# Performance work log

Hardware: AMD Instinct MI355X
Metric: run time of the kernel (lower is better)

Reference implementation:

```python
import jax, jax.numpy as jnp
import numpy as np

B, C, L, OUT = 64, 256, 4096, 256
EPS = 1e-5


def setup_inputs() -> dict:
    key = jax.random.key(0)
    ks = jax.random.split(key, 8)
    s = 1.0 / np.sqrt(C)
    return {
        "x": jax.random.normal(ks[0], (B, C, L), dtype=jnp.float32),
        "Wq": jax.random.normal(ks[1], (C, C), dtype=jnp.float32) * s,
        "Wk": jax.random.normal(ks[2], (C, C), dtype=jnp.float32) * s,
        "Wv": jax.random.normal(ks[3], (C, C), dtype=jnp.float32) * s,
        "Wc": jax.random.normal(ks[4], (C, C), dtype=jnp.float32) * s,
        "Wout": jax.random.normal(ks[5], (OUT, C), dtype=jnp.float32) * s,
        "gamma": jnp.ones((C,), dtype=jnp.float32),
        "beta": jnp.zeros((C,), dtype=jnp.float32),
    }


def _conv1x1(W, x):
    # 1x1 Conv1d, no bias: (O,C) x (B,C,L) -> (B,O,L)
    return jnp.einsum("oc,bcl->bol", W, x)


def reference(x, Wq, Wk, Wv, Wc, Wout, gamma, beta):
    q = _conv1x1(Wq, x)  # (B,C,L)
    k = _conv1x1(Wk, x)  # (B,C,L)
    v = _conv1x1(Wv, x)  # (B,C,L)
    # batch-wise attention: att[b,d,l] = sum_c q[b,c,l]*k[d,c,l] / sqrt(C)
    att = jnp.einsum("bcl,dcl->bdl", q, k) / jnp.sqrt(jnp.asarray(C, x.dtype))
    att = jax.nn.softmax(att, axis=1)  # softmax over the key-batch axis
    # virt[b,c,l] = sum_d att[b,d,l] * v[d,c,l]
    virt = jnp.einsum("bdl,dcl->bcl", att, v)
    # GroupNorm(1, C): normalize over (C,L) per sample, per-channel affine
    mean = jnp.mean(virt, axis=(1, 2), keepdims=True)
    var = jnp.var(virt, axis=(1, 2), keepdims=True)
    virt = (virt - mean) * jax.lax.rsqrt(var + EPS)
    virt = virt * gamma[None, :, None] + beta[None, :, None]
    virt = jax.nn.relu(virt)
    virt = _conv1x1(Wc, virt)
    # dropout is identity in eval mode
    y = x + virt
    return _conv1x1(Wout, y)
```

## Files before the change

kernel.cpp:

```cpp
#include <hip/hip_runtime.h>


typedef __attribute__((ext_vector_type(8))) short          v8s;
typedef __attribute__((ext_vector_type(8))) unsigned short v8u;
typedef __attribute__((ext_vector_type(4))) float          f32x4;

#define MFMA16(a, b, c) __builtin_amdgcn_mfma_f32_16x16x32_bf16((a), (b), (c), 0, 0, 0)

static __device__ __forceinline__ unsigned short f2bf(float f) {
  union { float f; unsigned u; } v; v.f = f;
  unsigned r = (v.u + 0x7FFFu + ((v.u >> 16) & 1u)) >> 16;
  return (unsigned short)r;
}
static __device__ __forceinline__ float bf2f(unsigned short h) {
  union { unsigned u; float f; } v; v.u = ((unsigned)h) << 16; return v.f;
}

__global__ void k_prep(const float* __restrict__ Wq, const float* __restrict__ Wk,
                       const float* __restrict__ Wv, const float* __restrict__ Wc,
                       const float* __restrict__ Wout,
                       unsigned short* __restrict__ Wtv,
                       unsigned short* __restrict__ Wout2,
                       float* __restrict__ stats) {
  int bid = blockIdx.x, j = threadIdx.x;
  if (bid < 256) {
    int i = bid;
    float acc = 0.f;
    for (int c = 0; c < 256; ++c) acc += Wq[c * 256 + i] * Wk[c * 256 + j];
    Wtv[i * 256 + j] = f2bf(acc * 0.0625f);
    Wtv[(256 + i) * 256 + j] = f2bf(Wv[i * 256 + j]);
  } else if (bid < 512) {
    int o = bid - 256;
    float acc = 0.f;
    for (int c = 0; c < 256; ++c) acc += Wout[o * 256 + c] * Wc[c * 256 + j];
    Wout2[o * 512 + 256 + j] = f2bf(acc);
    Wout2[o * 512 + j] = f2bf(Wout[o * 256 + j]);
  } else {
    stats[(bid - 512) * 256 + j] = 0.f;
  }
}

__global__ void k_transpose(const float* __restrict__ x, unsigned short* __restrict__ Xt) {
  __shared__ float tile[64 * 65];
  int bid = blockIdx.x;
  int b = bid >> 8, cb = (bid >> 6) & 3, lb = bid & 63;
  int c0 = cb * 64, l0 = lb * 64, t = threadIdx.x;
#pragma unroll
  for (int i = 0; i < 4; ++i) {
    int idx = i * 256 + t, r = idx >> 4, ch = idx & 15;
    float4 v = *(const float4*)(x + ((size_t)(b * 256 + c0 + r)) * 4096 + l0 + ch * 4);
    tile[r * 65 + ch * 4 + 0] = v.x; tile[r * 65 + ch * 4 + 1] = v.y;
    tile[r * 65 + ch * 4 + 2] = v.z; tile[r * 65 + ch * 4 + 3] = v.w;
  }
  __syncthreads();
#pragma unroll
  for (int i = 0; i < 2; ++i) {
    int idx = i * 256 + t, r = idx >> 3, ch = idx & 7;
    v8u o;
#pragma unroll
    for (int j = 0; j < 8; ++j) o[j] = f2bf(tile[(ch * 8 + j) * 65 + r]);
    *(v8u*)(Xt + ((size_t)(b * 4096 + l0 + r)) * 256 + c0 + ch * 8) = o;
  }
}

__global__ __launch_bounds__(512) void k_fused(const unsigned short* __restrict__ Xt,
                                               const unsigned short* __restrict__ Wtv,
                                               unsigned short* __restrict__ Virt,
                                               float* __restrict__ stats) {
  extern __shared__ char smem[];
  unsigned short* Xs  = (unsigned short*)(smem);
  unsigned short* Ts  = (unsigned short*)(smem + 33792);
  unsigned short* VTs = (unsigned short*)(smem + 67584);
  unsigned short* Ps  = (unsigned short*)(smem + 104448);
  float*          Ss  = (float*)(smem + 113664);
  float*          red = (float*)(smem + 130304);
  float*          rowv= (float*)(smem + 131328);

  int l = blockIdx.x, t = threadIdx.x, lane = t & 63, wv = t >> 6;
  int fr = lane & 15, kq = (lane >> 4) * 8, qr = (lane >> 4) * 4;

#pragma unroll
  for (int i = 0; i < 4; ++i) {
    int idx = i * 512 + t, r = idx >> 5, ch = idx & 31;
    *(v8u*)(Xs + r * 264 + ch * 8) = *(const v8u*)(Xt + ((size_t)(r * 4096 + l)) * 256 + ch * 8);
  }
  __syncthreads();

  {
    int n0 = wv * 64;
    f32x4 acc[4][4];
#pragma unroll
    for (int mi = 0; mi < 4; ++mi)
#pragma unroll
      for (int ni = 0; ni < 4; ++ni) acc[mi][ni] = (f32x4){0.f, 0.f, 0.f, 0.f};
#pragma unroll
    for (int kc = 0; kc < 8; ++kc) {
      v8s a[4], b[4];
#pragma unroll
      for (int mi = 0; mi < 4; ++mi) a[mi] = *(const v8s*)(Xs + (mi * 16 + fr) * 264 + kc * 32 + kq);
#pragma unroll
      for (int ni = 0; ni < 4; ++ni)
        b[ni] = *(const v8s*)(Wtv + (n0 + ni * 16 + fr) * 256 + kc * 32 + kq);
#pragma unroll
      for (int mi = 0; mi < 4; ++mi)
#pragma unroll
        for (int ni = 0; ni < 4; ++ni) acc[mi][ni] = MFMA16(a[mi], b[ni], acc[mi][ni]);
    }
    if (wv < 4) {
#pragma unroll
      for (int mi = 0; mi < 4; ++mi)
#pragma unroll
        for (int ni = 0; ni < 4; ++ni)
#pragma unroll
          for (int i = 0; i < 4; ++i)
            Ts[(mi * 16 + qr + i) * 264 + n0 + ni * 16 + fr] = f2bf(acc[mi][ni][i]);
    } else {
#pragma unroll
      for (int mi = 0; mi < 4; ++mi)
#pragma unroll
        for (int ni = 0; ni < 4; ++ni)
#pragma unroll
          for (int i = 0; i < 4; ++i)
            VTs[(n0 - 256 + ni * 16 + fr) * 72 + mi * 16 + qr + i] = f2bf(acc[mi][ni][i]);
    }
  }
  __syncthreads();

  {
    f32x4 acc[2];
    acc[0] = (f32x4){0.f, 0.f, 0.f, 0.f};
    acc[1] = (f32x4){0.f, 0.f, 0.f, 0.f};
    int tid0 = wv * 2;
#pragma unroll
    for (int kc = 0; kc < 8; ++kc) {
#pragma unroll
      for (int j = 0; j < 2; ++j) {
        int mi = (tid0 + j) >> 2, ni = (tid0 + j) & 3;
        v8s a = *(const v8s*)(Xs + (mi * 16 + fr) * 264 + kc * 32 + kq);
        v8s b = *(const v8s*)(Ts + (ni * 16 + fr) * 264 + kc * 32 + kq);
        acc[j] = MFMA16(a, b, acc[j]);
      }
    }
#pragma unroll
    for (int j = 0; j < 2; ++j) {
      int mi = (tid0 + j) >> 2, ni = (tid0 + j) & 3;
#pragma unroll
      for (int i = 0; i < 4; ++i)
        Ss[(mi * 16 + qr + i) * 65 + ni * 16 + fr] = acc[j][i];
    }
  }
  __syncthreads();

  if (t < 256) {
    int r = t >> 2, seg = t & 3;
    float pm = -1e30f;
    for (int j = seg * 16; j < seg * 16 + 16; ++j) pm = fmaxf(pm, Ss[r * 65 + j]);
    red[r * 4 + seg] = pm;
  }
  __syncthreads();
  if (t < 64) rowv[t] = fmaxf(fmaxf(red[t * 4], red[t * 4 + 1]), fmaxf(red[t * 4 + 2], red[t * 4 + 3]));
  __syncthreads();
  if (t < 256) {
    int r = t >> 2, seg = t & 3;
    float m = rowv[r], ps = 0.f;
    for (int j = seg * 16; j < seg * 16 + 16; ++j) {
      float e = __expf(Ss[r * 65 + j] - m);
      Ps[r * 72 + j] = f2bf(e);
      ps += e;
    }
    red[r * 4 + seg] = ps;
  }
  __syncthreads();
  if (t < 64) rowv[t] = 1.f / (red[t * 4] + red[t * 4 + 1] + red[t * 4 + 2] + red[t * 4 + 3]);
  __syncthreads();

  {
    int n0 = wv * 32;
    f32x4 acc[4][2];
#pragma unroll
    for (int mi = 0; mi < 4; ++mi) { acc[mi][0] = (f32x4){0,0,0,0}; acc[mi][1] = (f32x4){0,0,0,0}; }
#pragma unroll
    for (int kc = 0; kc < 2; ++kc) {
      v8s a[4], b[2];
#pragma unroll
      for (int mi = 0; mi < 4; ++mi) a[mi] = *(const v8s*)(Ps + (mi * 16 + fr) * 72 + kc * 32 + kq);
#pragma unroll
      for (int ni = 0; ni < 2; ++ni)
        b[ni] = *(const v8s*)(VTs + (n0 + ni * 16 + fr) * 72 + kc * 32 + kq);
#pragma unroll
      for (int mi = 0; mi < 4; ++mi)
#pragma unroll
        for (int ni = 0; ni < 2; ++ni) acc[mi][ni] = MFMA16(a[mi], b[ni], acc[mi][ni]);
    }
    __syncthreads();
#pragma unroll
    for (int mi = 0; mi < 4; ++mi)
#pragma unroll
      for (int i = 0; i < 4; ++i) {
        float inv = rowv[mi * 16 + qr + i];
#pragma unroll
        for (int ni = 0; ni < 2; ++ni)
          Ts[(mi * 16 + qr + i) * 264 + n0 + ni * 16 + fr] = f2bf(acc[mi][ni][i] * inv);
      }
  }
  __syncthreads();

  {
    int r = t >> 3, seg = t & 7;
    float s = 0.f, s2 = 0.f;
#pragma unroll
    for (int c4 = 0; c4 < 4; ++c4) {
      v8u v = *(const v8u*)(Ts + r * 264 + seg * 32 + c4 * 8);
#pragma unroll
      for (int j = 0; j < 8; ++j) { float f = bf2f(v[j]); s += f; s2 += f * f; }
      *(v8u*)(Virt + ((size_t)(r * 4096 + l)) * 256 + seg * 32 + c4 * 8) = v;
    }
#pragma unroll
    for (int o = 4; o > 0; o >>= 1) { s += __shfl_xor(s, o); s2 += __shfl_xor(s2, o); }
    if (seg == 0) {
      int slot = blockIdx.x & 31;
      atomicAdd(&stats[slot * 128 + r], s);
      atomicAdd(&stats[slot * 128 + 64 + r], s2);
    }
  }
}

__global__ void k_finalize(float* __restrict__ stats) {
  int t = threadIdx.x;
  if (t < 64) {
    float s = 0.f, s2 = 0.f;
    for (int sl = 0; sl < 32; ++sl) { s += stats[sl * 128 + t]; s2 += stats[sl * 128 + 64 + t]; }
    const float inv = 1.f / 1048576.f;
    float m = s * inv;
    float var = s2 * inv - m * m;
    stats[4096 + t] = m;
    stats[4160 + t] = rsqrtf(var + 1e-5f);
  }
}

__global__ void k_gemm_out(const unsigned short* __restrict__ Xt,
                           const unsigned short* __restrict__ Virt,
                           const unsigned short* __restrict__ Wout2,
                           const float* __restrict__ stats,
                           const float* __restrict__ gamma,
                           const float* __restrict__ beta,
                           float* __restrict__ out) {
  __shared__ unsigned short As[64 * 72];
  __shared__ unsigned short Bs[256 * 72];
  int t = threadIdx.x, lane = t & 63, wv = t >> 6;
  size_t t0 = (size_t)blockIdx.x * 64;
  int b = (int)(t0 >> 12);
  float mean = stats[4096 + b], rstd = stats[4160 + b];
  int n0 = wv * 64;
  f32x4 acc[4][4];
#pragma unroll
  for (int mi = 0; mi < 4; ++mi)
#pragma unroll
    for (int ni = 0; ni < 4; ++ni) acc[mi][ni] = (f32x4){0.f, 0.f, 0.f, 0.f};
  for (int kc = 0; kc < 8; ++kc) {
    __syncthreads();
#pragma unroll
    for (int i = 0; i < 2; ++i) {
      int idx = i * 256 + t, r = idx >> 3, ch = idx & 7;
      if (kc < 4) {
        *(v8u*)(As + r * 72 + ch * 8) = *(const v8u*)(Xt + (t0 + r) * 256 + kc * 64 + ch * 8);
      } else {
        v8u v = *(const v8u*)(Virt + (t0 + r) * 256 + (kc - 4) * 64 + ch * 8);
        int cb = (kc - 4) * 64 + ch * 8;
        float4 g0 = *(const float4*)(gamma + cb), g1 = *(const float4*)(gamma + cb + 4);
        float4 bb0 = *(const float4*)(beta + cb), bb1 = *(const float4*)(beta + cb + 4);
        float gs[8] = {g0.x, g0.y, g0.z, g0.w, g1.x, g1.y, g1.z, g1.w};
        float bs[8] = {bb0.x, bb0.y, bb0.z, bb0.w, bb1.x, bb1.y, bb1.z, bb1.w};
        v8u o;
#pragma unroll
        for (int j = 0; j < 8; ++j) {
          float z = (bf2f(v[j]) - mean) * rstd * gs[j] + bs[j];
          o[j] = f2bf(fmaxf(z, 0.f));
        }
        *(v8u*)(As + r * 72 + ch * 8) = o;
      }
    }
#pragma unroll
    for (int i = 0; i < 8; ++i) {
      int idx = i * 256 + t, r = idx >> 3, ch = idx & 7;
      *(v8u*)(Bs + r * 72 + ch * 8) = *(const v8u*)(Wout2 + r * 512 + kc * 64 + ch * 8);
    }
    __syncthreads();
#pragma unroll
    for (int ks = 0; ks < 2; ++ks) {
      int kq = ks * 32 + (lane >> 4) * 8;
      v8s a[4], bb[4];
#pragma unroll
      for (int mi = 0; mi < 4; ++mi) a[mi] = *(const v8s*)(As + (mi * 16 + (lane & 15)) * 72 + kq);
#pragma unroll
      for (int ni = 0; ni < 4; ++ni)
        bb[ni] = *(const v8s*)(Bs + (n0 + ni * 16 + (lane & 15)) * 72 + kq);
#pragma unroll
      for (int mi = 0; mi < 4; ++mi)
#pragma unroll
        for (int ni = 0; ni < 4; ++ni) acc[mi][ni] = MFMA16(a[mi], bb[ni], acc[mi][ni]);
    }
  }
  int qr = (lane >> 4) * 4, lbase = (int)(t0 & 4095);
#pragma unroll
  for (int mi = 0; mi < 4; ++mi)
#pragma unroll
    for (int ni = 0; ni < 4; ++ni)
#pragma unroll
      for (int i = 0; i < 4; ++i) {
        int ll = lbase + mi * 16 + qr + i;
        int o = n0 + ni * 16 + (lane & 15);
        out[((size_t)(b * 256 + o)) * 4096 + ll] = acc[mi][ni][i];
      }
}

extern "C" void kernel_launch(void* const* d_in, const int* in_sizes, int n_in,
                              void* d_out, int out_size, void* d_ws, size_t ws_size,
                              hipStream_t stream) {
  const float* x     = (const float*)d_in[0];
  const float* Wq    = (const float*)d_in[1];
  const float* Wk    = (const float*)d_in[2];
  const float* Wv    = (const float*)d_in[3];
  const float* Wc    = (const float*)d_in[4];
  const float* Wout  = (const float*)d_in[5];
  const float* gamma = (const float*)d_in[6];
  const float* beta  = (const float*)d_in[7];
  float* out = (float*)d_out;
  char* ws = (char*)d_ws;
  unsigned short* Xt   = (unsigned short*)(ws);
  unsigned short* Virt = (unsigned short*)(ws + 134217728ull);
  unsigned short* Wtv  = (unsigned short*)(ws + 268435456ull);
  unsigned short* W2   = (unsigned short*)(ws + 268697600ull);
  float* stats         = (float*)(ws + 268959744ull);

  static const int kFusedLds = 131584;
  hipFuncSetAttribute((const void*)k_fused, hipFuncAttributeMaxDynamicSharedMemorySize,
                      kFusedLds);

  k_prep<<<528, 256, 0, stream>>>(Wq, Wk, Wv, Wc, Wout, Wtv, W2, stats);
  k_transpose<<<16384, 256, 0, stream>>>(x, Xt);
  k_fused<<<4096, 512, kFusedLds, stream>>>(Xt, Wtv, Virt, stats);
  k_finalize<<<1, 64, 0, stream>>>(stats);
  k_gemm_out<<<4096, 256, 0, stream>>>(Xt, Virt, W2, stats, gamma, beta, out);
}
```

Before: 904.0 us.

## Shrink fused attention LDS footprint and keep softmax scores in registers

Restructures k_fused so the T projection and the V projection run as separate phases that reuse one LDS buffer, instead of holding T and V^T at once. The score tile now stays in MFMA accumulators, and the row max and sum are reduced with wave shuffles plus a small LDS exchange, which removes the fp32 score buffer and several barriers. LDS drops from about 131KB to about 81KB, and launch bounds now request more waves per SIMD, so occupancy can rise. In exchange the V projection is recomputed in a separate pass with different operand ordering, and tighter register bounds could cause spills.

```diff
diff --git a/kernel.cpp b/kernel.cpp
--- a/kernel.cpp
+++ b/kernel.cpp
@@ -3,6 +3,7 @@
 
 typedef __attribute__((ext_vector_type(8))) short          v8s;
 typedef __attribute__((ext_vector_type(8))) unsigned short v8u;
+typedef __attribute__((ext_vector_type(4))) unsigned short v4u;
 typedef __attribute__((ext_vector_type(4))) float          f32x4;
 
 #define MFMA16(a, b, c) __builtin_amdgcn_mfma_f32_16x16x32_bf16((a), (b), (c), 0, 0, 0)
@@ -63,20 +64,18 @@
   }
 }
 
-__global__ __launch_bounds__(512) void k_fused(const unsigned short* __restrict__ Xt,
-                                               const unsigned short* __restrict__ Wtv,
-                                               unsigned short* __restrict__ Virt,
-                                               float* __restrict__ stats) {
+__global__ __launch_bounds__(512, 4) void k_fused(const unsigned short* __restrict__ Xt,
+                                                  const unsigned short* __restrict__ Wtv,
+                                                  unsigned short* __restrict__ Virt,
+                                                  float* __restrict__ stats) {
   extern __shared__ char smem[];
   unsigned short* Xs  = (unsigned short*)(smem);
-  unsigned short* Ts  = (unsigned short*)(smem + 33792);
-  unsigned short* VTs = (unsigned short*)(smem + 67584);
-  unsigned short* Ps  = (unsigned short*)(smem + 104448);
-  float*          Ss  = (float*)(smem + 113664);
-  float*          red = (float*)(smem + 130304);
-  float*          rowv= (float*)(smem + 131328);
-
-  int l = blockIdx.x, t = threadIdx.x, lane = t & 63, wv = t >> 6;
+  unsigned short* Tb  = (unsigned short*)(smem + 33792);
+  unsigned short* Ps  = (unsigned short*)(smem + 70656);
+  float*          red = (float*)(smem + 79872);
+  float*          rowv= (float*)(smem + 80896);
+
+  int l = blockIdx.x, t = threadIdx.x, lane = t & 63, w = t >> 6;
   int fr = lane & 15, kq = (lane >> 4) * 8, qr = (lane >> 4) * 4;
 
 #pragma unroll
@@ -87,120 +86,142 @@
   __syncthreads();
 
   {
-    int n0 = wv * 64;
-    f32x4 acc[4][4];
+    int n0 = w * 32;
+    f32x4 acc[4][2];
 #pragma unroll
     for (int mi = 0; mi < 4; ++mi)
 #pragma unroll
-      for (int ni = 0; ni < 4; ++ni) acc[mi][ni] = (f32x4){0.f, 0.f, 0.f, 0.f};
+      for (int nj = 0; nj < 2; ++nj) acc[mi][nj] = (f32x4){0.f, 0.f, 0.f, 0.f};
 #pragma unroll
     for (int kc = 0; kc < 8; ++kc) {
-      v8s a[4], b[4];
+      v8s a[4], b[2];
 #pragma unroll
       for (int mi = 0; mi < 4; ++mi) a[mi] = *(const v8s*)(Xs + (mi * 16 + fr) * 264 + kc * 32 + kq);
 #pragma unroll
-      for (int ni = 0; ni < 4; ++ni)
-        b[ni] = *(const v8s*)(Wtv + (n0 + ni * 16 + fr) * 256 + kc * 32 + kq);
+      for (int nj = 0; nj < 2; ++nj)
+        b[nj] = *(const v8s*)(Wtv + ((size_t)(n0 + nj * 16 + fr)) * 256 + kc * 32 + kq);
 #pragma unroll
       for (int mi = 0; mi < 4; ++mi)
 #pragma unroll
-        for (int ni = 0; ni < 4; ++ni) acc[mi][ni] = MFMA16(a[mi], b[ni], acc[mi][ni]);
-    }
-    if (wv < 4) {
-#pragma unroll
-      for (int mi = 0; mi < 4; ++mi)
-#pragma unroll
-        for (int ni = 0; ni < 4; ++ni)
-#pragma unroll
-          for (int i = 0; i < 4; ++i)
-            Ts[(mi * 16 + qr + i) * 264 + n0 + ni * 16 + fr] = f2bf(acc[mi][ni][i]);
-    } else {
-#pragma unroll
-      for (int mi = 0; mi < 4; ++mi)
-#pragma unroll
-        for (int ni = 0; ni < 4; ++ni)
-#pragma unroll
-          for (int i = 0; i < 4; ++i)
-            VTs[(n0 - 256 + ni * 16 + fr) * 72 + mi * 16 + qr + i] = f2bf(acc[mi][ni][i]);
-    }
-  }
-  __syncthreads();
-
-  {
-    f32x4 acc[2];
-    acc[0] = (f32x4){0.f, 0.f, 0.f, 0.f};
-    acc[1] = (f32x4){0.f, 0.f, 0.f, 0.f};
-    int tid0 = wv * 2;
+        for (int nj = 0; nj < 2; ++nj) acc[mi][nj] = MFMA16(a[mi], b[nj], acc[mi][nj]);
+    }
+#pragma unroll
+    for (int mi = 0; mi < 4; ++mi)
+#pragma unroll
+      for (int nj = 0; nj < 2; ++nj)
+#pragma unroll
+        for (int i = 0; i < 4; ++i)
+          Tb[(mi * 16 + qr + i) * 264 + n0 + nj * 16 + fr] = f2bf(acc[mi][nj][i]);
+  }
+  __syncthreads();
+
+  int b0 = (w & 3) * 16, dp = (w >> 2) * 2, half = w >> 2;
+  f32x4 sacc[2];
+  sacc[0] = (f32x4){0.f, 0.f, 0.f, 0.f};
+  sacc[1] = (f32x4){0.f, 0.f, 0.f, 0.f};
+  {
 #pragma unroll
     for (int kc = 0; kc < 8; ++kc) {
+      v8s bb = *(const v8s*)(Xs + (b0 + fr) * 264 + kc * 32 + kq);
 #pragma unroll
       for (int j = 0; j < 2; ++j) {
-        int mi = (tid0 + j) >> 2, ni = (tid0 + j) & 3;
-        v8s a = *(const v8s*)(Xs + (mi * 16 + fr) * 264 + kc * 32 + kq);
-        v8s b = *(const v8s*)(Ts + (ni * 16 + fr) * 264 + kc * 32 + kq);
-        acc[j] = MFMA16(a, b, acc[j]);
-      }
-    }
+        v8s a = *(const v8s*)(Tb + ((dp + j) * 16 + fr) * 264 + kc * 32 + kq);
+        sacc[j] = MFMA16(a, bb, sacc[j]);
+      }
+    }
+    float pm = -1e30f;
+#pragma unroll
+    for (int j = 0; j < 2; ++j)
+#pragma unroll
+      for (int i = 0; i < 4; ++i) pm = fmaxf(pm, sacc[j][i]);
+    pm = fmaxf(pm, __shfl_xor(pm, 16));
+    pm = fmaxf(pm, __shfl_xor(pm, 32));
+    if (lane < 16) red[(b0 + lane) * 4 + half] = pm;
+  }
+  __syncthreads();
+
+  {
+    float m = fmaxf(red[(b0 + fr) * 4 + 0], red[(b0 + fr) * 4 + 1]);
+    float ps = 0.f;
 #pragma unroll
     for (int j = 0; j < 2; ++j) {
-      int mi = (tid0 + j) >> 2, ni = (tid0 + j) & 3;
-#pragma unroll
-      for (int i = 0; i < 4; ++i)
-        Ss[(mi * 16 + qr + i) * 65 + ni * 16 + fr] = acc[j][i];
-    }
-  }
-  __syncthreads();
-
-  if (t < 256) {
-    int r = t >> 2, seg = t & 3;
-    float pm = -1e30f;
-    for (int j = seg * 16; j < seg * 16 + 16; ++j) pm = fmaxf(pm, Ss[r * 65 + j]);
-    red[r * 4 + seg] = pm;
-  }
-  __syncthreads();
-  if (t < 64) rowv[t] = fmaxf(fmaxf(red[t * 4], red[t * 4 + 1]), fmaxf(red[t * 4 + 2], red[t * 4 + 3]));
-  __syncthreads();
-  if (t < 256) {
-    int r = t >> 2, seg = t & 3;
-    float m = rowv[r], ps = 0.f;
-    for (int j = seg * 16; j < seg * 16 + 16; ++j) {
-      float e = __expf(Ss[r * 65 + j] - m);
-      Ps[r * 72 + j] = f2bf(e);
-      ps += e;
-    }
-    red[r * 4 + seg] = ps;
-  }
-  __syncthreads();
-  if (t < 64) rowv[t] = 1.f / (red[t * 4] + red[t * 4 + 1] + red[t * 4 + 2] + red[t * 4 + 3]);
-  __syncthreads();
-
-  {
-    int n0 = wv * 32;
-    f32x4 acc[4][2];
-#pragma unroll
-    for (int mi = 0; mi < 4; ++mi) { acc[mi][0] = (f32x4){0,0,0,0}; acc[mi][1] = (f32x4){0,0,0,0}; }
+      v4u pk;
+#pragma unroll
+      for (int i = 0; i < 4; ++i) {
+        float e = __expf(sacc[j][i] - m);
+        ps += e;
+        pk[i] = f2bf(e);
+      }
+      *(v4u*)(Ps + (b0 + fr) * 72 + (dp + j) * 16 + qr) = pk;
+    }
+    ps += __shfl_xor(ps, 16);
+    ps += __shfl_xor(ps, 32);
+    if (lane < 16) red[(b0 + lane) * 4 + 2 + half] = ps;
+  }
+
+  {
+    int c0 = w * 32;
+    f32x4 vacc[2][4];
+#pragma unroll
+    for (int ci = 0; ci < 2; ++ci)
+#pragma unroll
+      for (int di = 0; di < 4; ++di) vacc[ci][di] = (f32x4){0.f, 0.f, 0.f, 0.f};
+#pragma unroll
+    for (int kc = 0; kc < 8; ++kc) {
+      v8s a[2], b[4];
+#pragma unroll
+      for (int ci = 0; ci < 2; ++ci)
+        a[ci] = *(const v8s*)(Wtv + ((size_t)(256 + c0 + ci * 16 + fr)) * 256 + kc * 32 + kq);
+#pragma unroll
+      for (int di = 0; di < 4; ++di) b[di] = *(const v8s*)(Xs + (di * 16 + fr) * 264 + kc * 32 + kq);
+#pragma unroll
+      for (int ci = 0; ci < 2; ++ci)
+#pragma unroll
+        for (int di = 0; di < 4; ++di) vacc[ci][di] = MFMA16(a[ci], b[di], vacc[ci][di]);
+    }
+#pragma unroll
+    for (int ci = 0; ci < 2; ++ci)
+#pragma unroll
+      for (int di = 0; di < 4; ++di)
+#pragma unroll
+        for (int i = 0; i < 4; ++i)
+          Tb[(c0 + ci * 16 + qr + i) * 72 + di * 16 + fr] = f2bf(vacc[ci][di][i]);
+  }
+  __syncthreads();
+
+  if (t < 64) rowv[t] = 1.f / (red[t * 4 + 2] + red[t * 4 + 3]);
+
+  f32x4 pacc[4][2];
+#pragma unroll
+  for (int mi = 0; mi < 4; ++mi) { pacc[mi][0] = (f32x4){0,0,0,0}; pacc[mi][1] = (f32x4){0,0,0,0}; }
+  {
+    int n0 = w * 32;
 #pragma unroll
     for (int kc = 0; kc < 2; ++kc) {
       v8s a[4], b[2];
 #pragma unroll
       for (int mi = 0; mi < 4; ++mi) a[mi] = *(const v8s*)(Ps + (mi * 16 + fr) * 72 + kc * 32 + kq);
 #pragma unroll
-      for (int ni = 0; ni < 2; ++ni)
-        b[ni] = *(const v8s*)(VTs + (n0 + ni * 16 + fr) * 72 + kc * 32 + kq);
+      for (int nj = 0; nj < 2; ++nj)
+        b[nj] = *(const v8s*)(Tb + (n0 + nj * 16 + fr) * 72 + kc * 32 + kq);
 #pragma unroll
       for (int mi = 0; mi < 4; ++mi)
 #pragma unroll
-        for (int ni = 0; ni < 2; ++ni) acc[mi][ni] = MFMA16(a[mi], b[ni], acc[mi][ni]);
-    }
-    __syncthreads();
+        for (int nj = 0; nj < 2; ++nj) pacc[mi][nj] = MFMA16(a[mi], b[nj], pacc[mi][nj]);
+    }
+  }
+  __syncthreads();
+
+  {
+    int n0 = w * 32;
 #pragma unroll
     for (int mi = 0; mi < 4; ++mi)
 #pragma unroll
       for (int i = 0; i < 4; ++i) {
         float inv = rowv[mi * 16 + qr + i];
 #pragma unroll
-        for (int ni = 0; ni < 2; ++ni)
-          Ts[(mi * 16 + qr + i) * 264 + n0 + ni * 16 + fr] = f2bf(acc[mi][ni][i] * inv);
+        for (int nj = 0; nj < 2; ++nj)
+          Tb[(mi * 16 + qr + i) * 264 + n0 + nj * 16 + fr] = f2bf(pacc[mi][nj][i] * inv);
       }
   }
   __syncthreads();
@@ -210,7 +231,7 @@
     float s = 0.f, s2 = 0.f;
 #pragma unroll
     for (int c4 = 0; c4 < 4; ++c4) {
-      v8u v = *(const v8u*)(Ts + r * 264 + seg * 32 + c4 * 8);
+      v8u v = *(const v8u*)(Tb + r * 264 + seg * 32 + c4 * 8);
 #pragma unroll
       for (int j = 0; j < 8; ++j) { float f = bf2f(v[j]); s += f; s2 += f * f; }
       *(v8u*)(Virt + ((size_t)(r * 4096 + l)) * 256 + seg * 32 + c4 * 8) = v;
@@ -333,7 +354,7 @@
   unsigned short* W2   = (unsigned short*)(ws + 268697600ull);
   float* stats         = (float*)(ws + 268959744ull);
 
-  static const int kFusedLds = 131584;
+  static const int kFusedLds = 81152;
   hipFuncSetAttribute((const void*)k_fused, hipFuncAttributeMaxDynamicSharedMemorySize,
                       kFusedLds);
 
```

After: 863.8 us. 1.05x faster.
